# Kernel tuning notes

Measured on AMD Instinct MI355X. Metric: run time of the kernel, lower is better.

The kernel has to match this reference:

```python
import jax, jax.numpy as jnp
import numpy as np

FACTOR = 0.25  # lossFunc(factor=0.25)


def _argmax_coords(x):
    # x: [B, H, W] -> [B, 2] float coords (row, col) of the max element.
    # Matches (p == p.max()).nonzero().float() when the max is unique
    # (true a.s. for continuous random inputs).
    B, H, W = x.shape
    idx = jnp.argmax(x.reshape(B, H * W), axis=-1)
    return jnp.stack([idx // W, idx % W], axis=-1).astype(x.dtype)


def setup_inputs() -> dict:
    key = jax.random.key(0)
    k1, k2 = jax.random.split(key)
    pred = jax.random.normal(k1, (64, 512, 512), dtype=jnp.float32)
    label = jax.random.normal(k2, (64, 1, 512, 512), dtype=jnp.float32)
    return {"pred": pred, "label": label}


def reference(pred, label):
    label0 = label[:, 0]                      # [B, H, W]
    B = pred.shape[0]
    # Vectorized replacement of the per-sample Python loop:
    cp = _argmax_coords(pred)                 # [B, 2]
    cl = _argmax_coords(label0)               # [B, 2]
    # sum-reduced MSE over coordinates (size_average=False), summed over batch
    idx_loss = jnp.sum((cp - cl) ** 2)
    # sum-reduced MSE over all elements
    mse_loss = jnp.sum((pred - label0) ** 2)
    # alpha comes from .item() in torch -> a constant scalar
    alpha = jnp.where(idx_loss != 0, mse_loss / idx_loss, jnp.asarray(1.0, pred.dtype))
    alpha = jax.lax.stop_gradient(alpha)
    loss = (mse_loss + FACTOR * alpha * idx_loss) / B
    return loss
```

## Files before the change

kernel.cpp:

```cpp
#include <hip/hip_runtime.h>
#include <math.h>

#define HW 262144
#define BPB 32
#define CHUNK 8192
#define NBLK (64 * BPB)

#define GL2LDS(g, l)                                                      \
    __builtin_amdgcn_global_load_lds(                                     \
        (const __attribute__((address_space(1))) void*)(g),               \
        (__attribute__((address_space(3))) void*)(l), 16, 0, 0)

__device__ __forceinline__ unsigned int fmono(float f) {
    unsigned int u = __float_as_uint(f);
    return (u & 0x80000000u) ? ~u : (u | 0x80000000u);
}

__global__ __launch_bounds__(256) void reduce_kernel(
    const float* __restrict__ pred, const float* __restrict__ label,
    unsigned long long* __restrict__ pblk, unsigned long long* __restrict__ lblk,
    float* __restrict__ sblk)
{
    __shared__ __align__(16) float lds[2 * CHUNK];

    const int bi = blockIdx.x;
    const int b = bi >> 5;
    const int chunk = bi & (BPB - 1);
    const float* pbase = pred  + (size_t)b * HW + (size_t)chunk * CHUNK;
    const float* lbase = label + (size_t)b * HW + (size_t)chunk * CHUNK;
    const int t = threadIdx.x;
    const int wave = t >> 6, lane = t & 63;
    const unsigned int base = (unsigned int)chunk * CHUNK;

    {
        const int seg = wave * 2048 + lane * 4;
        const float* pg = pbase + seg;
        const float* lg = lbase + seg;
        float* pl = lds + wave * 2048;
        float* ll = lds + CHUNK + wave * 2048;
#pragma unroll
        for (int j = 0; j < 8; ++j) {
            GL2LDS(pg + j * 256, pl + j * 256);
            GL2LDS(lg + j * 256, ll + j * 256);
        }
    }
    __syncthreads();

    const float4* lp4 = (const float4*)lds;
    const float4* ll4 = (const float4*)(lds + CHUNK);

    float sumsq = 0.0f;
    float pmax = -INFINITY, lmax = -INFINITY;
    unsigned int pidx = 0, lidx = 0;

#pragma unroll
    for (int i = 0; i < 8; ++i) {
        const float4 p = lp4[i * 256 + t];
        const float4 l = ll4[i * 256 + t];
        const unsigned int e = base + ((unsigned int)(i * 256 + t)) * 4u;
        float d;
        d = p.x - l.x; sumsq += d * d;
        d = p.y - l.y; sumsq += d * d;
        d = p.z - l.z; sumsq += d * d;
        d = p.w - l.w; sumsq += d * d;
        if (p.x > pmax) { pmax = p.x; pidx = e;      }
        if (p.y > pmax) { pmax = p.y; pidx = e + 1u; }
        if (p.z > pmax) { pmax = p.z; pidx = e + 2u; }
        if (p.w > pmax) { pmax = p.w; pidx = e + 3u; }
        if (l.x > lmax) { lmax = l.x; lidx = e;      }
        if (l.y > lmax) { lmax = l.y; lidx = e + 1u; }
        if (l.z > lmax) { lmax = l.z; lidx = e + 2u; }
        if (l.w > lmax) { lmax = l.w; lidx = e + 3u; }
    }

    unsigned long long ppk = ((unsigned long long)fmono(pmax) << 32) | (unsigned long long)(0xFFFFFFFFu - pidx);
    unsigned long long lpk = ((unsigned long long)fmono(lmax) << 32) | (unsigned long long)(0xFFFFFFFFu - lidx);

    for (int off = 32; off > 0; off >>= 1) {
        sumsq += __shfl_down(sumsq, off);
        unsigned long long o;
        o = __shfl_down(ppk, off); if (o > ppk) ppk = o;
        o = __shfl_down(lpk, off); if (o > lpk) lpk = o;
    }

    __shared__ float s_sum[4];
    __shared__ unsigned long long s_pp[4], s_lp[4];
    if (lane == 0) { s_sum[wave] = sumsq; s_pp[wave] = ppk; s_lp[wave] = lpk; }
    __syncthreads();
    if (t == 0) {
        float s = s_sum[0] + s_sum[1] + s_sum[2] + s_sum[3];
        unsigned long long Pk = s_pp[0], Lk = s_lp[0];
#pragma unroll
        for (int i = 1; i < 4; ++i) {
            if (s_pp[i] > Pk) Pk = s_pp[i];
            if (s_lp[i] > Lk) Lk = s_lp[i];
        }
        pblk[bi] = Pk;
        lblk[bi] = Lk;
        sblk[bi] = s;
    }
}

__global__ __launch_bounds__(1024) void finalize_kernel(
    const unsigned long long* __restrict__ pblk,
    const unsigned long long* __restrict__ lblk,
    const float* __restrict__ sblk,
    float* __restrict__ out)
{
    const int t = threadIdx.x;

    float s = sblk[t] + sblk[t + 1024];
    for (int off = 32; off > 0; off >>= 1) s += __shfl_down(s, off);
    __shared__ float ss[16];
    const int wave = t >> 6;
    if ((t & 63) == 0) ss[wave] = s;

    const int batch = t >> 4, j = t & 15;
    unsigned long long Pv = pblk[batch * 32 + j];
    unsigned long long o  = pblk[batch * 32 + j + 16];
    if (o > Pv) Pv = o;
    unsigned long long Lv = lblk[batch * 32 + j];
    o = lblk[batch * 32 + j + 16];
    if (o > Lv) Lv = o;
    for (int off = 8; off > 0; off >>= 1) {
        o = __shfl_down(Pv, off, 16); if (o > Pv) Pv = o;
        o = __shfl_down(Lv, off, 16); if (o > Lv) Lv = o;
    }
    __shared__ float dd[64];
    if (j == 0) {
        const unsigned int ip = 0xFFFFFFFFu - (unsigned int)(Pv & 0xFFFFFFFFull);
        const unsigned int il = 0xFFFFFFFFu - (unsigned int)(Lv & 0xFFFFFFFFull);
        const float rp = (float)(ip >> 9), cp = (float)(ip & 511u);
        const float rl = (float)(il >> 9), cl = (float)(il & 511u);
        dd[batch] = (rp - rl) * (rp - rl) + (cp - cl) * (cp - cl);
    }
    __syncthreads();
    if (t < 64) {
        float d = dd[t];
        for (int off = 32; off > 0; off >>= 1) d += __shfl_down(d, off);
        if (t == 0) {
            float m = 0.0f;
#pragma unroll
            for (int i = 0; i < 16; ++i) m += ss[i];
            const float alpha = (d != 0.0f) ? (m / d) : 1.0f;
            out[0] = (m + 0.25f * alpha * d) / 64.0f;
        }
    }
}

extern "C" void kernel_launch(void* const* d_in, const int* in_sizes, int n_in,
                              void* d_out, int out_size, void* d_ws, size_t ws_size,
                              hipStream_t stream) {
    const float* pred  = (const float*)d_in[0];
    const float* label = (const float*)d_in[1];
    float* out = (float*)d_out;

    unsigned long long* pblk = (unsigned long long*)d_ws;
    unsigned long long* lblk = pblk + NBLK;
    float* sblk = (float*)(lblk + NBLK);

    reduce_kernel<<<dim3(NBLK), dim3(256), 0, stream>>>(pred, label, pblk, lblk, sblk);
    finalize_kernel<<<dim3(1), dim3(1024), 0, stream>>>(pblk, lblk, sblk, out);
}
```

Measured before the change: 146.4 us.

## Fuse finalize into reduce kernel via last-block atomic and use direct nontemporal loads

Merges the two kernels into one. The last block to finish, detected with an atomic counter, performs the final reduction, which removes the second kernel launch. A memset is added to reset the counter on each call. The global-to-LDS async staging is also replaced with direct nontemporal float4 loads into registers, dropping the LDS buffer and a barrier. The cost is that the memset runs as a separate stream operation and the serial tail now runs in a 256-thread block instead of 1024 threads.

```diff
diff --git a/kernel.cpp b/kernel.cpp
--- a/kernel.cpp
+++ b/kernel.cpp
@@ -6,48 +6,27 @@
 #define CHUNK 8192
 #define NBLK (64 * BPB)
 
-#define GL2LDS(g, l)                                                      \
-    __builtin_amdgcn_global_load_lds(                                     \
-        (const __attribute__((address_space(1))) void*)(g),               \
-        (__attribute__((address_space(3))) void*)(l), 16, 0, 0)
+typedef float f4 __attribute__((ext_vector_type(4)));
 
 __device__ __forceinline__ unsigned int fmono(float f) {
     unsigned int u = __float_as_uint(f);
     return (u & 0x80000000u) ? ~u : (u | 0x80000000u);
 }
 
-__global__ __launch_bounds__(256) void reduce_kernel(
+__global__ __launch_bounds__(256) void loss_kernel(
     const float* __restrict__ pred, const float* __restrict__ label,
     unsigned long long* __restrict__ pblk, unsigned long long* __restrict__ lblk,
-    float* __restrict__ sblk)
+    float* __restrict__ sblk, unsigned int* __restrict__ cnt,
+    float* __restrict__ out)
 {
-    __shared__ __align__(16) float lds[2 * CHUNK];
-
     const int bi = blockIdx.x;
     const int b = bi >> 5;
     const int chunk = bi & (BPB - 1);
-    const float* pbase = pred  + (size_t)b * HW + (size_t)chunk * CHUNK;
-    const float* lbase = label + (size_t)b * HW + (size_t)chunk * CHUNK;
+    const f4* p4 = (const f4*)(pred + (size_t)b * HW) + (size_t)chunk * (CHUNK / 4);
+    const f4* l4 = (const f4*)(label + (size_t)b * HW) + (size_t)chunk * (CHUNK / 4);
     const int t = threadIdx.x;
     const int wave = t >> 6, lane = t & 63;
     const unsigned int base = (unsigned int)chunk * CHUNK;
-
-    {
-        const int seg = wave * 2048 + lane * 4;
-        const float* pg = pbase + seg;
-        const float* lg = lbase + seg;
-        float* pl = lds + wave * 2048;
-        float* ll = lds + CHUNK + wave * 2048;
-#pragma unroll
-        for (int j = 0; j < 8; ++j) {
-            GL2LDS(pg + j * 256, pl + j * 256);
-            GL2LDS(lg + j * 256, ll + j * 256);
-        }
-    }
-    __syncthreads();
-
-    const float4* lp4 = (const float4*)lds;
-    const float4* ll4 = (const float4*)(lds + CHUNK);
 
     float sumsq = 0.0f;
     float pmax = -INFINITY, lmax = -INFINITY;
@@ -55,22 +34,22 @@
 
 #pragma unroll
     for (int i = 0; i < 8; ++i) {
-        const float4 p = lp4[i * 256 + t];
-        const float4 l = ll4[i * 256 + t];
+        const f4 p = __builtin_nontemporal_load(p4 + i * 256 + t);
+        const f4 l = __builtin_nontemporal_load(l4 + i * 256 + t);
         const unsigned int e = base + ((unsigned int)(i * 256 + t)) * 4u;
         float d;
-        d = p.x - l.x; sumsq += d * d;
-        d = p.y - l.y; sumsq += d * d;
-        d = p.z - l.z; sumsq += d * d;
-        d = p.w - l.w; sumsq += d * d;
-        if (p.x > pmax) { pmax = p.x; pidx = e;      }
-        if (p.y > pmax) { pmax = p.y; pidx = e + 1u; }
-        if (p.z > pmax) { pmax = p.z; pidx = e + 2u; }
-        if (p.w > pmax) { pmax = p.w; pidx = e + 3u; }
-        if (l.x > lmax) { lmax = l.x; lidx = e;      }
-        if (l.y > lmax) { lmax = l.y; lidx = e + 1u; }
-        if (l.z > lmax) { lmax = l.z; lidx = e + 2u; }
-        if (l.w > lmax) { lmax = l.w; lidx = e + 3u; }
+        d = p[0] - l[0]; sumsq += d * d;
+        d = p[1] - l[1]; sumsq += d * d;
+        d = p[2] - l[2]; sumsq += d * d;
+        d = p[3] - l[3]; sumsq += d * d;
+        if (p[0] > pmax) { pmax = p[0]; pidx = e;      }
+        if (p[1] > pmax) { pmax = p[1]; pidx = e + 1u; }
+        if (p[2] > pmax) { pmax = p[2]; pidx = e + 2u; }
+        if (p[3] > pmax) { pmax = p[3]; pidx = e + 3u; }
+        if (l[0] > lmax) { lmax = l[0]; lidx = e;      }
+        if (l[1] > lmax) { lmax = l[1]; lidx = e + 1u; }
+        if (l[2] > lmax) { lmax = l[2]; lidx = e + 2u; }
+        if (l[3] > lmax) { lmax = l[3]; lidx = e + 3u; }
     }
 
     unsigned long long ppk = ((unsigned long long)fmono(pmax) << 32) | (unsigned long long)(0xFFFFFFFFu - pidx);
@@ -85,6 +64,7 @@
 
     __shared__ float s_sum[4];
     __shared__ unsigned long long s_pp[4], s_lp[4];
+    __shared__ unsigned int s_last;
     if (lane == 0) { s_sum[wave] = sumsq; s_pp[wave] = ppk; s_lp[wave] = lpk; }
     __syncthreads();
     if (t == 0) {
@@ -98,33 +78,31 @@
         pblk[bi] = Pk;
         lblk[bi] = Lk;
         sblk[bi] = s;
+        __threadfence();
+        s_last = (atomicAdd(cnt, 1u) == NBLK - 1u);
     }
-}
+    __syncthreads();
+    if (!s_last) return;
 
-__global__ __launch_bounds__(1024) void finalize_kernel(
-    const unsigned long long* __restrict__ pblk,
-    const unsigned long long* __restrict__ lblk,
-    const float* __restrict__ sblk,
-    float* __restrict__ out)
-{
-    const int t = threadIdx.x;
+    __threadfence();
 
-    float s = sblk[t] + sblk[t + 1024];
+    float s = 0.0f;
+#pragma unroll
+    for (int k = 0; k < 8; ++k) s = s + sblk[t + k * 256];
     for (int off = 32; off > 0; off >>= 1) s += __shfl_down(s, off);
-    __shared__ float ss[16];
-    const int wave = t >> 6;
-    if ((t & 63) == 0) ss[wave] = s;
+    __shared__ float ss[4];
+    if (lane == 0) ss[wave] = s;
 
-    const int batch = t >> 4, j = t & 15;
-    unsigned long long Pv = pblk[batch * 32 + j];
-    unsigned long long o  = pblk[batch * 32 + j + 16];
-    if (o > Pv) Pv = o;
-    unsigned long long Lv = lblk[batch * 32 + j];
-    o = lblk[batch * 32 + j + 16];
-    if (o > Lv) Lv = o;
-    for (int off = 8; off > 0; off >>= 1) {
-        o = __shfl_down(Pv, off, 16); if (o > Pv) Pv = o;
-        o = __shfl_down(Lv, off, 16); if (o > Lv) Lv = o;
+    const int batch = t >> 2, j = t & 3;
+    unsigned long long Pv = 0ull, Lv = 0ull, o;
+#pragma unroll
+    for (int k = 0; k < 8; ++k) {
+        o = pblk[batch * 32 + j + k * 4]; if (o > Pv) Pv = o;
+        o = lblk[batch * 32 + j + k * 4]; if (o > Lv) Lv = o;
+    }
+    for (int off = 2; off > 0; off >>= 1) {
+        o = __shfl_down(Pv, off, 4); if (o > Pv) Pv = o;
+        o = __shfl_down(Lv, off, 4); if (o > Lv) Lv = o;
     }
     __shared__ float dd[64];
     if (j == 0) {
@@ -139,9 +117,7 @@
         float d = dd[t];
         for (int off = 32; off > 0; off >>= 1) d += __shfl_down(d, off);
         if (t == 0) {
-            float m = 0.0f;
-#pragma unroll
-            for (int i = 0; i < 16; ++i) m += ss[i];
+            const float m = ss[0] + ss[1] + ss[2] + ss[3];
             const float alpha = (d != 0.0f) ? (m / d) : 1.0f;
             out[0] = (m + 0.25f * alpha * d) / 64.0f;
         }
@@ -158,7 +134,9 @@
     unsigned long long* pblk = (unsigned long long*)d_ws;
     unsigned long long* lblk = pblk + NBLK;
     float* sblk = (float*)(lblk + NBLK);
+    unsigned int* cnt = (unsigned int*)(sblk + NBLK);
 
-    reduce_kernel<<<dim3(NBLK), dim3(256), 0, stream>>>(pred, label, pblk, lblk, sblk);
-    finalize_kernel<<<dim3(1), dim3(1024), 0, stream>>>(pblk, lblk, sblk, out);
+    (void)hipMemsetAsync(cnt, 0, sizeof(unsigned int), stream);
+
+    loss_kernel<<<dim3(NBLK), dim3(256), 0, stream>>>(pred, label, pblk, lblk, sblk, cnt, out);
 }
```

After: 235.6 us. 61.0% more time.
